# Kernel tuning notes

Hardware: AMD Instinct MI355X
Metric: run time of the kernel (lower is better)

Reference implementation:

```python
import jax, jax.numpy as jnp
import numpy as np

N, C_S, C_Z, H, D = 512, 384, 128, 16, 24  # c_hidden per head
EPS = 1e-5

def _ln(x, g, b):
    m = jnp.mean(x, axis=-1, keepdims=True)
    v = jnp.mean(jnp.square(x - m), axis=-1, keepdims=True)
    return (x - m) * jax.lax.rsqrt(v + EPS) * g + b

def setup_inputs() -> dict:
    key = jax.random.key(0)
    ks = jax.random.split(key, 12)
    s = lambda fan: 1.0 / np.sqrt(fan)
    return {
        "a": jax.random.normal(ks[0], (1, N, C_S), jnp.float32),
        "z": jax.random.normal(ks[1], (1, N, N, C_Z), jnp.float32),
        "g_a": jnp.ones((C_S,), jnp.float32),
        "b_a": jnp.zeros((C_S,), jnp.float32),
        "g_z": jnp.ones((C_Z,), jnp.float32),
        "b_z": jnp.zeros((C_Z,), jnp.float32),
        "Wz": jax.random.normal(ks[2], (C_Z, H), jnp.float32) * s(C_Z),
        "bz": jnp.zeros((H,), jnp.float32),
        "Wq": jax.random.normal(ks[3], (C_S, H * D), jnp.float32) * s(C_S),
        "Wk": jax.random.normal(ks[4], (C_S, H * D), jnp.float32) * s(C_S),
        "Wv": jax.random.normal(ks[5], (C_S, H * D), jnp.float32) * s(C_S),
        "Wg": jax.random.normal(ks[6], (C_S, H * D), jnp.float32) * s(C_S),
        "bg": jnp.zeros((H * D,), jnp.float32),
        "Wo": jax.random.normal(ks[7], (H * D, C_S), jnp.float32) * s(H * D),
        "bo": jnp.zeros((C_S,), jnp.float32),
    }

def reference(a, z, g_a, b_a, g_z, b_z, Wz, bz, Wq, Wk, Wv, Wg, bg, Wo, bo):
    B = a.shape[0]
    a_n = _ln(a, g_a, b_a)                       # [B,N,C_S]
    z_n = _ln(z, g_z, b_z)                       # [B,N,N,C_Z]
    # linear_z then permute(0,3,1,2): [B,N,N,H] -> [B,H,N,N]
    pair_bias = jnp.einsum('bijc,ch->bhij', z_n, Wz) + bz[None, :, None, None]
    q = (a_n @ Wq).reshape(B, N, H, D) * (1.0 / np.sqrt(D))
    k = (a_n @ Wk).reshape(B, N, H, D)
    v = (a_n @ Wv).reshape(B, N, H, D)
    scores = jnp.einsum('bqhd,bkhd->bhqk', q, k) + pair_bias
    p = jax.nn.softmax(scores, axis=-1)
    o = jnp.einsum('bhqk,bkhd->bqhd', p, v)      # [B,N,H,D]
    g = jax.nn.sigmoid(a_n @ Wg + bg).reshape(B, N, H, D)
    o = (o * g).reshape(B, N, H * D)
    return o @ Wo + bo                            # [B,N,C_S]
```

## Files before the change

### kernel.cpp

```cpp
#include <hip/hip_runtime.h>
#include <math.h>

#define N 512
#define CS 384
#define CZ 128
#define NH 16
#define DH 24
#define HD 384
#define NN (N*N)
#define EPS 1e-5f

#define OFF_AN   0
#define OFF_QT   196608
#define OFF_KT   393216
#define OFF_VT   589824
#define OFF_GT   786432
#define OFF_OG   983040
#define OFF_WZ2  1179648
#define OFF_SH   1181696
#define OFF_BH   1181712
#define OFF_BIAS 1181728

__global__ void __launch_bounds__(256) ln_prep_kernel(const float* __restrict__ a, const float* __restrict__ g_a,
                                                      const float* __restrict__ b_a, float* __restrict__ an_out,
                                                      const float* __restrict__ g_z, const float* __restrict__ lnb_z,
                                                      const float* __restrict__ Wz, const float* __restrict__ bz,
                                                      float* __restrict__ wz2, float* __restrict__ sh,
                                                      float* __restrict__ bh) {
    __shared__ float ls[NH][17], lb[NH][17];
    __shared__ float l1[4], l2[4];
    const int t = threadIdx.x;
    if (blockIdx.x == 256) {
        for (int i = t; i < NH * CZ; i += 256) {
            int h = i >> 7, c = i & (CZ - 1);
            wz2[h * CZ + c] = g_z[c] * Wz[c * NH + h];
        }
        int h = t >> 4, seg = t & 15;
        float s = 0.f, b = 0.f;
        #pragma unroll
        for (int i = 0; i < 8; ++i) {
            int c = seg * 8 + i;
            float w = Wz[c * NH + h];
            s += g_z[c] * w;
            b += lnb_z[c] * w;
        }
        ls[h][seg] = s; lb[h][seg] = b;
        __syncthreads();
        if (t < NH) {
            float ss = 0.f, bb = 0.f;
            #pragma unroll
            for (int i = 0; i < 16; ++i) { ss += ls[t][i]; bb += lb[t][i]; }
            sh[t] = ss;
            bh[t] = bb + bz[t];
        }
        return;
    }
    const int half = t >> 7;
    const int tr = t & 127;
    const int r = blockIdx.x * 2 + half;
    const float* row = a + r * CS;
    float x0 = row[tr], x1 = row[tr + 128], x2 = row[tr + 256];
    float s1 = x0 + x1 + x2;
    float s2 = x0 * x0 + x1 * x1 + x2 * x2;
    #pragma unroll
    for (int m = 1; m < 64; m <<= 1) {
        s1 += __shfl_xor(s1, m, 64);
        s2 += __shfl_xor(s2, m, 64);
    }
    if ((t & 63) == 0) { l1[t >> 6] = s1; l2[t >> 6] = s2; }
    __syncthreads();
    s1 = l1[half * 2] + l1[half * 2 + 1];
    s2 = l2[half * 2] + l2[half * 2 + 1];
    float mu = s1 * (1.f / CS);
    float var = s2 * (1.f / CS) - mu * mu;
    float rs = rsqrtf(var + EPS);
    float* an = an_out + r * CS;
    an[tr]       = (x0 - mu) * rs * g_a[tr]       + b_a[tr];
    an[tr + 128] = (x1 - mu) * rs * g_a[tr + 128] + b_a[tr + 128];
    an[tr + 256] = (x2 - mu) * rs * g_a[tr + 256] + b_a[tr + 256];
}

__global__ void __launch_bounds__(256) qkvg_kernel(const float* __restrict__ Wq, const float* __restrict__ Wk,
                                                   const float* __restrict__ Wv, const float* __restrict__ Wg,
                                                   const float* __restrict__ bg, const float* __restrict__ an,
                                                   float* __restrict__ qt, float* __restrict__ kt,
                                                   float* __restrict__ vt, float* __restrict__ gt) {
    const int lane = threadIdx.x & 63;
    const int w = __builtin_amdgcn_readfirstlane(threadIdx.x >> 6);
    const int strip = blockIdx.x * 4 + w;
    const int n0 = strip * 8;
    const int sel = n0 / HD;
    const int col = n0 % HD;
    const float* Wm = (sel == 0) ? Wq : (sel == 1) ? Wk : (sel == 2) ? Wv : Wg;
    const int m = blockIdx.y * 64 + lane;
    const float* arow = an + m * CS;
    float acc[8];
    #pragma unroll
    for (int j = 0; j < 8; ++j) acc[j] = 0.f;
    for (int kb = 0; kb < CS; kb += 32) {
        float4 av[8];
        #pragma unroll
        for (int i = 0; i < 8; ++i) av[i] = ((const float4*)(arow + kb))[i];
        #pragma unroll
        for (int i = 0; i < 8; ++i) {
            const float* wr = Wm + (kb + i * 4) * HD + col;
            #pragma unroll
            for (int j = 0; j < 8; ++j) {
                acc[j] += av[i].x * wr[j];
                acc[j] += av[i].y * wr[HD + j];
                acc[j] += av[i].z * wr[2 * HD + j];
                acc[j] += av[i].w * wr[3 * HD + j];
            }
        }
    }
    float* dst = (sel == 0) ? qt : (sel == 1) ? kt : (sel == 2) ? vt : gt;
    if (sel == 3) {
        #pragma unroll
        for (int j = 0; j < 8; ++j) acc[j] = 1.f / (1.f + __expf(-(acc[j] + bg[col + j])));
    } else if (sel == 0) {
        #pragma unroll
        for (int j = 0; j < 8; ++j) acc[j] *= 0.20412414523193153f;
    }
    #pragma unroll
    for (int j = 0; j < 8; ++j) {
        int c = col + j;
        int h = c / DH, d = c % DH;
        dst[(h * N + m) * DH + d] = acc[j];
    }
}

__global__ void __launch_bounds__(256, 4) pairbias_kernel(const float* __restrict__ z,
                                                          const float* __restrict__ wz2,
                                                          const float* __restrict__ sh,
                                                          const float* __restrict__ bh,
                                                          float* __restrict__ bias) {
    __shared__ float4 lz[64 * 32];
    const int t = threadIdx.x;
    const int l = t & 63;
    const int w = __builtin_amdgcn_readfirstlane(t >> 6);
    const int h0 = w * 4;
    const int row0 = blockIdx.x * 64;

    const float4* zsrc = (const float4*)(z + (size_t)row0 * CZ);
    #pragma unroll
    for (int i = 0; i < 8; ++i) {
        const int g4 = i * 256 + t;
        float4 v = zsrc[g4];
        const int r = g4 >> 5, cc = g4 & 31;
        lz[r * 32 + (cc ^ (r & 31))] = v;
    }
    __syncthreads();

    const unsigned base = (unsigned)(l * 512 + ((l & 31) << 4));
    const char* lzb = (const char*)lz;
    float s1 = 0.f, s2 = 0.f;
    float dots[4];
    #pragma unroll
    for (int j = 0; j < 4; ++j) dots[j] = 0.f;
    #pragma unroll
    for (int cc = 0; cc < 32; ++cc) {
        float4 v = *(const float4*)(lzb + (base ^ (unsigned)(cc << 4)));
        s1 += v.x + v.y + v.z + v.w;
        s2 += v.x * v.x + v.y * v.y + v.z * v.z + v.w * v.w;
        #pragma unroll
        for (int j = 0; j < 4; ++j) {
            const float4 wv = ((const float4*)(wz2 + (h0 + j) * CZ))[cc];
            dots[j] += v.x * wv.x + v.y * wv.y + v.z * wv.z + v.w * wv.w;
        }
    }
    const float mu = s1 * (1.f / CZ);
    const float var = s2 * (1.f / CZ) - mu * mu;
    const float rr = rsqrtf(var + EPS);
    const int row = row0 + l;
    #pragma unroll
    for (int j = 0; j < 4; ++j)
        bias[(h0 + j) * NN + row] = rr * (dots[j] - mu * sh[h0 + j]) + bh[h0 + j];
}

__global__ void __launch_bounds__(256) attn_kernel(const float* __restrict__ qt, const float* __restrict__ kt,
                                                   const float* __restrict__ vt, const float* __restrict__ gt,
                                                   const float* __restrict__ bias, float* __restrict__ og) {
    const int lane = threadIdx.x & 63;
    const int w = __builtin_amdgcn_readfirstlane(threadIdx.x >> 6);
    const int qhalf = lane >> 5;
    const int klane = lane & 31;
    const int h = blockIdx.y;
    const int q = blockIdx.x * 8 + w * 2 + qhalf;
    const float* qT = qt + h * N * DH;
    const float* kT = kt + h * N * DH;
    const float* vT = vt + h * N * DH;

    float qv[DH];
    #pragma unroll
    for (int d6 = 0; d6 < 6; ++d6) {
        float4 t4 = ((const float4*)(qT + q * DH))[d6];
        qv[d6 * 4 + 0] = t4.x; qv[d6 * 4 + 1] = t4.y; qv[d6 * 4 + 2] = t4.z; qv[d6 * 4 + 3] = t4.w;
    }
    float sc[16];
    #pragma unroll
    for (int t = 0; t < 16; ++t) {
        const int kk = t * 32 + klane;
        const float4* kr = (const float4*)(kT + kk * DH);
        float4 k0 = kr[0], k1 = kr[1], k2 = kr[2], k3 = kr[3], k4 = kr[4], k5 = kr[5];
        float s = qv[0]*k0.x + qv[1]*k0.y + qv[2]*k0.z + qv[3]*k0.w
                + qv[4]*k1.x + qv[5]*k1.y + qv[6]*k1.z + qv[7]*k1.w
                + qv[8]*k2.x + qv[9]*k2.y + qv[10]*k2.z + qv[11]*k2.w
                + qv[12]*k3.x + qv[13]*k3.y + qv[14]*k3.z + qv[15]*k3.w
                + qv[16]*k4.x + qv[17]*k4.y + qv[18]*k4.z + qv[19]*k4.w
                + qv[20]*k5.x + qv[21]*k5.y + qv[22]*k5.z + qv[23]*k5.w;
        sc[t] = s + bias[h * NN + q * N + kk];
    }
    float mx = sc[0];
    #pragma unroll
    for (int t = 1; t < 16; ++t) mx = fmaxf(mx, sc[t]);
    #pragma unroll
    for (int m = 1; m < 32; m <<= 1) mx = fmaxf(mx, __shfl_xor(mx, m, 64));
    float sum = 0.f;
    #pragma unroll
    for (int t = 0; t < 16; ++t) { sc[t] = __expf(sc[t] - mx); sum += sc[t]; }
    #pragma unroll
    for (int m = 1; m < 32; m <<= 1) sum += __shfl_xor(sum, m, 64);
    float inv = 1.f / sum;
    #pragma unroll
    for (int t = 0; t < 16; ++t) sc[t] *= inv;
    float acc[DH];
    #pragma unroll
    for (int d = 0; d < DH; ++d) acc[d] = 0.f;
    #pragma unroll
    for (int t = 0; t < 16; ++t) {
        const int kk = t * 32 + klane;
        const float4* vr = (const float4*)(vT + kk * DH);
        float4 v0 = vr[0], v1 = vr[1], v2 = vr[2], v3 = vr[3], v4 = vr[4], v5 = vr[5];
        float p = sc[t];
        acc[0] += p*v0.x;  acc[1] += p*v0.y;  acc[2] += p*v0.z;  acc[3] += p*v0.w;
        acc[4] += p*v1.x;  acc[5] += p*v1.y;  acc[6] += p*v1.z;  acc[7] += p*v1.w;
        acc[8] += p*v2.x;  acc[9] += p*v2.y;  acc[10] += p*v2.z; acc[11] += p*v2.w;
        acc[12] += p*v3.x; acc[13] += p*v3.y; acc[14] += p*v3.z; acc[15] += p*v3.w;
        acc[16] += p*v4.x; acc[17] += p*v4.y; acc[18] += p*v4.z; acc[19] += p*v4.w;
        acc[20] += p*v5.x; acc[21] += p*v5.y; acc[22] += p*v5.z; acc[23] += p*v5.w;
    }
    #pragma unroll
    for (int m = 1; m < 32; m <<= 1) {
        #pragma unroll
        for (int d = 0; d < DH; ++d) acc[d] += __shfl_xor(acc[d], m, 64);
    }
    float o = 0.f;
    #pragma unroll
    for (int d = 0; d < DH; ++d) o = (klane == d) ? acc[d] : o;
    if (klane < DH) {
        float g = gt[h * N * DH + q * DH + klane];
        og[q * HD + h * DH + klane] = o * g;
    }
}

__global__ void __launch_bounds__(256) out_gemm_kernel(const float* __restrict__ Wo, const float* __restrict__ bo,
                                                       const float* __restrict__ og, float* __restrict__ out) {
    const int lane = threadIdx.x & 63;
    const int w = __builtin_amdgcn_readfirstlane(threadIdx.x >> 6);
    const int strip = blockIdx.x * 4 + w;
    const int c0 = strip * 4;
    const int m = blockIdx.y * 64 + lane;
    const float* orow = og + m * HD;
    float acc[4];
    #pragma unroll
    for (int j = 0; j < 4; ++j) acc[j] = 0.f;
    for (int kb = 0; kb < HD; kb += 32) {
        float4 av[8];
        #pragma unroll
        for (int i = 0; i < 8; ++i) av[i] = ((const float4*)(orow + kb))[i];
        #pragma unroll
        for (int i = 0; i < 8; ++i) {
            const float* wr = Wo + (kb + i * 4) * CS + c0;
            #pragma unroll
            for (int j = 0; j < 4; ++j) {
                acc[j] += av[i].x * wr[j];
                acc[j] += av[i].y * wr[CS + j];
                acc[j] += av[i].z * wr[2 * CS + j];
                acc[j] += av[i].w * wr[3 * CS + j];
            }
        }
    }
    #pragma unroll
    for (int j = 0; j < 4; ++j) out[m * CS + c0 + j] = acc[j] + bo[c0 + j];
}

extern "C" void kernel_launch(void* const* d_in, const int* in_sizes, int n_in,
                              void* d_out, int out_size, void* d_ws, size_t ws_size,
                              hipStream_t stream) {
    const float* a    = (const float*)d_in[0];
    const float* z    = (const float*)d_in[1];
    const float* g_a  = (const float*)d_in[2];
    const float* b_a  = (const float*)d_in[3];
    const float* g_z  = (const float*)d_in[4];
    const float* b_z  = (const float*)d_in[5];
    const float* Wz   = (const float*)d_in[6];
    const float* bz   = (const float*)d_in[7];
    const float* Wq   = (const float*)d_in[8];
    const float* Wk   = (const float*)d_in[9];
    const float* Wv   = (const float*)d_in[10];
    const float* Wg   = (const float*)d_in[11];
    const float* bg   = (const float*)d_in[12];
    const float* Wo   = (const float*)d_in[13];
    const float* bo   = (const float*)d_in[14];
    float* ws  = (float*)d_ws;
    float* out = (float*)d_out;

    float* an   = ws + OFF_AN;
    float* qt   = ws + OFF_QT;
    float* kt   = ws + OFF_KT;
    float* vt   = ws + OFF_VT;
    float* gt   = ws + OFF_GT;
    float* ogp  = ws + OFF_OG;
    float* wz2  = ws + OFF_WZ2;
    float* shp  = ws + OFF_SH;
    float* bhp  = ws + OFF_BH;
    float* bias = ws + OFF_BIAS;

    hipLaunchKernelGGL(ln_prep_kernel, dim3(257),    dim3(256), 0, stream,
                       a, g_a, b_a, an, g_z, b_z, Wz, bz, wz2, shp, bhp);
    hipLaunchKernelGGL(qkvg_kernel,    dim3(48, 8),  dim3(256), 0, stream,
                       Wq, Wk, Wv, Wg, bg, an, qt, kt, vt, gt);
    hipLaunchKernelGGL(pairbias_kernel, dim3(4096),  dim3(256), 0, stream,
                       z, wz2, shp, bhp, bias);
    hipLaunchKernelGGL(attn_kernel,    dim3(64, 16), dim3(256), 0, stream,
                       qt, kt, vt, gt, bias, ogp);
    hipLaunchKernelGGL(out_gemm_kernel, dim3(24, 8), dim3(256), 0, stream,
                       Wo, bo, ogp, out);
}
```

Baseline: 334.0 us.

## Merge QKVG projection into pair-bias kernel and shrink output GEMM strips

Combines the QKVG projection and the pair-bias computation into one launch. Every ninth block does a narrower 6-column projection strip and the other blocks do pair-bias rows, so the small compute-bound GEMM overlaps the bandwidth-bound z streaming. The output GEMM now computes 2 columns per wave over a 1D grid of 384 blocks, giving more blocks for better occupancy. This saves one launch and the idle tail between kernels, at the cost of branch divergence per block and less weight reuse per thread.

```diff
diff --git a/kernel.cpp b/kernel.cpp
--- a/kernel.cpp
+++ b/kernel.cpp
@@ -80,66 +80,69 @@
     an[tr + 256] = (x2 - mu) * rs * g_a[tr + 256] + b_a[tr + 256];
 }
 
-__global__ void __launch_bounds__(256) qkvg_kernel(const float* __restrict__ Wq, const float* __restrict__ Wk,
-                                                   const float* __restrict__ Wv, const float* __restrict__ Wg,
-                                                   const float* __restrict__ bg, const float* __restrict__ an,
-                                                   float* __restrict__ qt, float* __restrict__ kt,
-                                                   float* __restrict__ vt, float* __restrict__ gt) {
-    const int lane = threadIdx.x & 63;
-    const int w = __builtin_amdgcn_readfirstlane(threadIdx.x >> 6);
-    const int strip = blockIdx.x * 4 + w;
-    const int n0 = strip * 8;
-    const int sel = n0 / HD;
-    const int col = n0 % HD;
-    const float* Wm = (sel == 0) ? Wq : (sel == 1) ? Wk : (sel == 2) ? Wv : Wg;
-    const int m = blockIdx.y * 64 + lane;
-    const float* arow = an + m * CS;
-    float acc[8];
-    #pragma unroll
-    for (int j = 0; j < 8; ++j) acc[j] = 0.f;
-    for (int kb = 0; kb < CS; kb += 32) {
-        float4 av[8];
-        #pragma unroll
-        for (int i = 0; i < 8; ++i) av[i] = ((const float4*)(arow + kb))[i];
-        #pragma unroll
-        for (int i = 0; i < 8; ++i) {
-            const float* wr = Wm + (kb + i * 4) * HD + col;
-            #pragma unroll
-            for (int j = 0; j < 8; ++j) {
-                acc[j] += av[i].x * wr[j];
-                acc[j] += av[i].y * wr[HD + j];
-                acc[j] += av[i].z * wr[2 * HD + j];
-                acc[j] += av[i].w * wr[3 * HD + j];
+__global__ void __launch_bounds__(256, 4) qp2_kernel(const float* __restrict__ z,
+                                                     const float* __restrict__ wz2,
+                                                     const float* __restrict__ sh,
+                                                     const float* __restrict__ bh,
+                                                     float* __restrict__ bias,
+                                                     const float* __restrict__ Wq, const float* __restrict__ Wk,
+                                                     const float* __restrict__ Wv, const float* __restrict__ Wg,
+                                                     const float* __restrict__ bg, const float* __restrict__ an,
+                                                     float* __restrict__ qt, float* __restrict__ kt,
+                                                     float* __restrict__ vt, float* __restrict__ gt) {
+    __shared__ float4 lz[64 * 32];
+    const int b = blockIdx.x;
+    const int t = threadIdx.x;
+    const int lane = t & 63;
+    const int w = __builtin_amdgcn_readfirstlane(t >> 6);
+    if (b % 9 == 8) {
+        const int bq = b / 9;
+        const int wid = bq * 4 + w;
+        const int strip = wid >> 3;
+        const int mb = wid & 7;
+        const int n0 = strip * 6;
+        const int sel = n0 / HD;
+        const int col = n0 - sel * HD;
+        const float* Wm = (sel == 0) ? Wq : (sel == 1) ? Wk : (sel == 2) ? Wv : Wg;
+        const int m = mb * 64 + lane;
+        const float* arow = an + m * CS;
+        float acc[6];
+        #pragma unroll
+        for (int j = 0; j < 6; ++j) acc[j] = 0.f;
+        for (int kb = 0; kb < CS; kb += 32) {
+            float4 av[8];
+            #pragma unroll
+            for (int i = 0; i < 8; ++i) av[i] = ((const float4*)(arow + kb))[i];
+            #pragma unroll
+            for (int i = 0; i < 8; ++i) {
+                const float* wr = Wm + (kb + i * 4) * HD + col;
+                #pragma unroll
+                for (int j = 0; j < 6; ++j) {
+                    acc[j] += av[i].x * wr[j];
+                    acc[j] += av[i].y * wr[HD + j];
+                    acc[j] += av[i].z * wr[2 * HD + j];
+                    acc[j] += av[i].w * wr[3 * HD + j];
+                }
             }
         }
-    }
-    float* dst = (sel == 0) ? qt : (sel == 1) ? kt : (sel == 2) ? vt : gt;
-    if (sel == 3) {
-        #pragma unroll
-        for (int j = 0; j < 8; ++j) acc[j] = 1.f / (1.f + __expf(-(acc[j] + bg[col + j])));
-    } else if (sel == 0) {
-        #pragma unroll
-        for (int j = 0; j < 8; ++j) acc[j] *= 0.20412414523193153f;
-    }
-    #pragma unroll
-    for (int j = 0; j < 8; ++j) {
-        int c = col + j;
-        int h = c / DH, d = c % DH;
-        dst[(h * N + m) * DH + d] = acc[j];
-    }
-}
-
-__global__ void __launch_bounds__(256, 4) pairbias_kernel(const float* __restrict__ z,
-                                                          const float* __restrict__ wz2,
-                                                          const float* __restrict__ sh,
-                                                          const float* __restrict__ bh,
-                                                          float* __restrict__ bias) {
-    __shared__ float4 lz[64 * 32];
-    const int t = threadIdx.x;
+        float* dst = (sel == 0) ? qt : (sel == 1) ? kt : (sel == 2) ? vt : gt;
+        if (sel == 3) {
+            #pragma unroll
+            for (int j = 0; j < 6; ++j) acc[j] = 1.f / (1.f + __expf(-(acc[j] + bg[col + j])));
+        } else if (sel == 0) {
+            #pragma unroll
+            for (int j = 0; j < 6; ++j) acc[j] *= 0.20412414523193153f;
+        }
+        const int h = col / DH, d0 = col - h * DH;
+        float* dp = dst + (h * N + m) * DH + d0;
+        #pragma unroll
+        for (int j = 0; j < 6; ++j) dp[j] = acc[j];
+        return;
+    }
+    const int pb = b - (b + 1) / 9;
     const int l = t & 63;
-    const int w = __builtin_amdgcn_readfirstlane(t >> 6);
     const int h0 = w * 4;
-    const int row0 = blockIdx.x * 64;
+    const int row0 = pb * 64;
 
     const float4* zsrc = (const float4*)(z + (size_t)row0 * CZ);
     #pragma unroll
@@ -257,13 +260,14 @@
                                                        const float* __restrict__ og, float* __restrict__ out) {
     const int lane = threadIdx.x & 63;
     const int w = __builtin_amdgcn_readfirstlane(threadIdx.x >> 6);
-    const int strip = blockIdx.x * 4 + w;
-    const int c0 = strip * 4;
-    const int m = blockIdx.y * 64 + lane;
+    const int wid = blockIdx.x * 4 + w;
+    const int strip = wid >> 3;
+    const int mb = wid & 7;
+    const int c0 = strip * 2;
+    const int m = mb * 64 + lane;
     const float* orow = og + m * HD;
-    float acc[4];
-    #pragma unroll
-    for (int j = 0; j < 4; ++j) acc[j] = 0.f;
+    float acc[2];
+    acc[0] = 0.f; acc[1] = 0.f;
     for (int kb = 0; kb < HD; kb += 32) {
         float4 av[8];
         #pragma unroll
@@ -272,7 +276,7 @@
         for (int i = 0; i < 8; ++i) {
             const float* wr = Wo + (kb + i * 4) * CS + c0;
             #pragma unroll
-            for (int j = 0; j < 4; ++j) {
+            for (int j = 0; j < 2; ++j) {
                 acc[j] += av[i].x * wr[j];
                 acc[j] += av[i].y * wr[CS + j];
                 acc[j] += av[i].z * wr[2 * CS + j];
@@ -281,7 +285,7 @@
         }
     }
     #pragma unroll
-    for (int j = 0; j < 4; ++j) out[m * CS + c0 + j] = acc[j] + bo[c0 + j];
+    for (int j = 0; j < 2; ++j) out[m * CS + c0 + j] = acc[j] + bo[c0 + j];
 }
 
 extern "C" void kernel_launch(void* const* d_in, const int* in_sizes, int n_in,
@@ -318,12 +322,11 @@
 
     hipLaunchKernelGGL(ln_prep_kernel, dim3(257),    dim3(256), 0, stream,
                        a, g_a, b_a, an, g_z, b_z, Wz, bz, wz2, shp, bhp);
-    hipLaunchKernelGGL(qkvg_kernel,    dim3(48, 8),  dim3(256), 0, stream,
+    hipLaunchKernelGGL(qp2_kernel,     dim3(4608),   dim3(256), 0, stream,
+                       z, wz2, shp, bhp, bias,
                        Wq, Wk, Wv, Wg, bg, an, qt, kt, vt, gt);
-    hipLaunchKernelGGL(pairbias_kernel, dim3(4096),  dim3(256), 0, stream,
-                       z, wz2, shp, bhp, bias);
     hipLaunchKernelGGL(attn_kernel,    dim3(64, 16), dim3(256), 0, stream,
                        qt, kt, vt, gt, bias, ogp);
-    hipLaunchKernelGGL(out_gemm_kernel, dim3(24, 8), dim3(256), 0, stream,
+    hipLaunchKernelGGL(out_gemm_kernel, dim3(384),   dim3(256), 0, stream,
                        Wo, bo, ogp, out);
 }
```

Result: slower. 404.3 us (+21.0%).

## Stage K/V and GEMM activations in swizzled LDS, use online softmax in attention

Applied to the files above, without the earlier changes.

The attention kernel now loads 128-key tiles of K and V cooperatively into XOR-swizzled shared memory and uses an online (running max/sum) softmax across four tiles, instead of each wave reading K/V rows straight from global memory. The QKVG and output GEMMs stage the activation tile in swizzled LDS and halve the columns per wave, doubling the grid to raise parallelism. The intent is to cut redundant global loads and register pressure, at the cost of extra barriers and rescaling work per tile.

```diff
diff --git a/kernel.cpp b/kernel.cpp
--- a/kernel.cpp
+++ b/kernel.cpp
@@ -85,27 +85,38 @@
                                                    const float* __restrict__ bg, const float* __restrict__ an,
                                                    float* __restrict__ qt, float* __restrict__ kt,
                                                    float* __restrict__ vt, float* __restrict__ gt) {
-    const int lane = threadIdx.x & 63;
-    const int w = __builtin_amdgcn_readfirstlane(threadIdx.x >> 6);
-    const int strip = blockIdx.x * 4 + w;
-    const int n0 = strip * 8;
+    __shared__ float4 lan[64 * 8];
+    const int t = threadIdx.x;
+    const int lane = t & 63;
+    const int w = __builtin_amdgcn_readfirstlane(t >> 6);
+    const int s = blockIdx.x * 4 + w;
+    const int n0 = s * 4;
     const int sel = n0 / HD;
-    const int col = n0 % HD;
+    const int col = n0 - sel * HD;
     const float* Wm = (sel == 0) ? Wq : (sel == 1) ? Wk : (sel == 2) ? Wv : Wg;
-    const int m = blockIdx.y * 64 + lane;
-    const float* arow = an + m * CS;
-    float acc[8];
-    #pragma unroll
-    for (int j = 0; j < 8; ++j) acc[j] = 0.f;
+    const int m0 = blockIdx.y * 64;
+    const int m = m0 + lane;
+    const float4* an4 = (const float4*)an;
+    float acc[4];
+    #pragma unroll
+    for (int j = 0; j < 4; ++j) acc[j] = 0.f;
     for (int kb = 0; kb < CS; kb += 32) {
+        __syncthreads();
+        #pragma unroll
+        for (int i = 0; i < 2; ++i) {
+            const int idx = i * 256 + t;
+            const int r = idx >> 3, c = idx & 7;
+            lan[(r << 3) + (c ^ (r & 7))] = an4[(size_t)(m0 + r) * 96 + (kb >> 2) + c];
+        }
+        __syncthreads();
         float4 av[8];
         #pragma unroll
-        for (int i = 0; i < 8; ++i) av[i] = ((const float4*)(arow + kb))[i];
+        for (int i = 0; i < 8; ++i) av[i] = lan[(lane << 3) + (i ^ (lane & 7))];
         #pragma unroll
         for (int i = 0; i < 8; ++i) {
             const float* wr = Wm + (kb + i * 4) * HD + col;
             #pragma unroll
-            for (int j = 0; j < 8; ++j) {
+            for (int j = 0; j < 4; ++j) {
                 acc[j] += av[i].x * wr[j];
                 acc[j] += av[i].y * wr[HD + j];
                 acc[j] += av[i].z * wr[2 * HD + j];
@@ -116,17 +127,15 @@
     float* dst = (sel == 0) ? qt : (sel == 1) ? kt : (sel == 2) ? vt : gt;
     if (sel == 3) {
         #pragma unroll
-        for (int j = 0; j < 8; ++j) acc[j] = 1.f / (1.f + __expf(-(acc[j] + bg[col + j])));
+        for (int j = 0; j < 4; ++j) acc[j] = 1.f / (1.f + __expf(-(acc[j] + bg[col + j])));
     } else if (sel == 0) {
         #pragma unroll
-        for (int j = 0; j < 8; ++j) acc[j] *= 0.20412414523193153f;
-    }
-    #pragma unroll
-    for (int j = 0; j < 8; ++j) {
-        int c = col + j;
-        int h = c / DH, d = c % DH;
-        dst[(h * N + m) * DH + d] = acc[j];
-    }
+        for (int j = 0; j < 4; ++j) acc[j] *= 0.20412414523193153f;
+    }
+    const int h = col / DH, d0 = col - h * DH;
+    float* dp = dst + (h * N + m) * DH + d0;
+    #pragma unroll
+    for (int j = 0; j < 4; ++j) dp[j] = acc[j];
 }
 
 __global__ void __launch_bounds__(256, 4) pairbias_kernel(const float* __restrict__ z,
@@ -177,18 +186,22 @@
         bias[(h0 + j) * NN + row] = rr * (dots[j] - mu * sh[h0 + j]) + bh[h0 + j];
 }
 
-__global__ void __launch_bounds__(256) attn_kernel(const float* __restrict__ qt, const float* __restrict__ kt,
-                                                   const float* __restrict__ vt, const float* __restrict__ gt,
-                                                   const float* __restrict__ bias, float* __restrict__ og) {
-    const int lane = threadIdx.x & 63;
-    const int w = __builtin_amdgcn_readfirstlane(threadIdx.x >> 6);
+__global__ void __launch_bounds__(256, 4) attn_kernel(const float* __restrict__ qt, const float* __restrict__ kt,
+                                                      const float* __restrict__ vt, const float* __restrict__ gt,
+                                                      const float* __restrict__ bias, float* __restrict__ og) {
+    __shared__ float4 lzK[128 * 8];
+    __shared__ float4 lzV[128 * 8];
+    const int t = threadIdx.x;
+    const int lane = t & 63;
+    const int w = __builtin_amdgcn_readfirstlane(t >> 6);
     const int qhalf = lane >> 5;
     const int klane = lane & 31;
     const int h = blockIdx.y;
     const int q = blockIdx.x * 8 + w * 2 + qhalf;
     const float* qT = qt + h * N * DH;
-    const float* kT = kt + h * N * DH;
-    const float* vT = vt + h * N * DH;
+    const float4* kT4 = (const float4*)(kt + h * N * DH);
+    const float4* vT4 = (const float4*)(vt + h * N * DH);
+    const float* brow = bias + h * NN + q * N;
 
     float qv[DH];
     #pragma unroll
@@ -196,83 +209,115 @@
         float4 t4 = ((const float4*)(qT + q * DH))[d6];
         qv[d6 * 4 + 0] = t4.x; qv[d6 * 4 + 1] = t4.y; qv[d6 * 4 + 2] = t4.z; qv[d6 * 4 + 3] = t4.w;
     }
-    float sc[16];
-    #pragma unroll
-    for (int t = 0; t < 16; ++t) {
-        const int kk = t * 32 + klane;
-        const float4* kr = (const float4*)(kT + kk * DH);
-        float4 k0 = kr[0], k1 = kr[1], k2 = kr[2], k3 = kr[3], k4 = kr[4], k5 = kr[5];
-        float s = qv[0]*k0.x + qv[1]*k0.y + qv[2]*k0.z + qv[3]*k0.w
-                + qv[4]*k1.x + qv[5]*k1.y + qv[6]*k1.z + qv[7]*k1.w
-                + qv[8]*k2.x + qv[9]*k2.y + qv[10]*k2.z + qv[11]*k2.w
-                + qv[12]*k3.x + qv[13]*k3.y + qv[14]*k3.z + qv[15]*k3.w
-                + qv[16]*k4.x + qv[17]*k4.y + qv[18]*k4.z + qv[19]*k4.w
-                + qv[20]*k5.x + qv[21]*k5.y + qv[22]*k5.z + qv[23]*k5.w;
-        sc[t] = s + bias[h * NN + q * N + kk];
-    }
-    float mx = sc[0];
-    #pragma unroll
-    for (int t = 1; t < 16; ++t) mx = fmaxf(mx, sc[t]);
-    #pragma unroll
-    for (int m = 1; m < 32; m <<= 1) mx = fmaxf(mx, __shfl_xor(mx, m, 64));
-    float sum = 0.f;
-    #pragma unroll
-    for (int t = 0; t < 16; ++t) { sc[t] = __expf(sc[t] - mx); sum += sc[t]; }
-    #pragma unroll
-    for (int m = 1; m < 32; m <<= 1) sum += __shfl_xor(sum, m, 64);
-    float inv = 1.f / sum;
-    #pragma unroll
-    for (int t = 0; t < 16; ++t) sc[t] *= inv;
+    float m_run = -1e30f, l_run = 0.f;
     float acc[DH];
     #pragma unroll
     for (int d = 0; d < DH; ++d) acc[d] = 0.f;
-    #pragma unroll
-    for (int t = 0; t < 16; ++t) {
-        const int kk = t * 32 + klane;
-        const float4* vr = (const float4*)(vT + kk * DH);
-        float4 v0 = vr[0], v1 = vr[1], v2 = vr[2], v3 = vr[3], v4 = vr[4], v5 = vr[5];
-        float p = sc[t];
-        acc[0] += p*v0.x;  acc[1] += p*v0.y;  acc[2] += p*v0.z;  acc[3] += p*v0.w;
-        acc[4] += p*v1.x;  acc[5] += p*v1.y;  acc[6] += p*v1.z;  acc[7] += p*v1.w;
-        acc[8] += p*v2.x;  acc[9] += p*v2.y;  acc[10] += p*v2.z; acc[11] += p*v2.w;
-        acc[12] += p*v3.x; acc[13] += p*v3.y; acc[14] += p*v3.z; acc[15] += p*v3.w;
-        acc[16] += p*v4.x; acc[17] += p*v4.y; acc[18] += p*v4.z; acc[19] += p*v4.w;
-        acc[20] += p*v5.x; acc[21] += p*v5.y; acc[22] += p*v5.z; acc[23] += p*v5.w;
+
+    for (int tile = 0; tile < 4; ++tile) {
+        __syncthreads();
+        const int kt0 = tile * 128;
+        #pragma unroll
+        for (int i = 0; i < 3; ++i) {
+            const int idx = i * 256 + t;
+            const int r = idx / 6, c = idx - r * 6;
+            const int slot = (r << 3) + (c ^ (r & 7));
+            lzK[slot] = kT4[kt0 * 6 + idx];
+            lzV[slot] = vT4[kt0 * 6 + idx];
+        }
+        __syncthreads();
+        float sc[4];
+        #pragma unroll
+        for (int j = 0; j < 4; ++j) {
+            const int kk = j * 32 + klane;
+            const float4* kr = lzK + (kk << 3);
+            const int x = kk & 7;
+            float4 k0 = kr[0 ^ x], k1 = kr[1 ^ x], k2 = kr[2 ^ x],
+                   k3 = kr[3 ^ x], k4 = kr[4 ^ x], k5 = kr[5 ^ x];
+            float s = qv[0]*k0.x + qv[1]*k0.y + qv[2]*k0.z + qv[3]*k0.w
+                    + qv[4]*k1.x + qv[5]*k1.y + qv[6]*k1.z + qv[7]*k1.w
+                    + qv[8]*k2.x + qv[9]*k2.y + qv[10]*k2.z + qv[11]*k2.w
+                    + qv[12]*k3.x + qv[13]*k3.y + qv[14]*k3.z + qv[15]*k3.w
+                    + qv[16]*k4.x + qv[17]*k4.y + qv[18]*k4.z + qv[19]*k4.w
+                    + qv[20]*k5.x + qv[21]*k5.y + qv[22]*k5.z + qv[23]*k5.w;
+            sc[j] = s + brow[kt0 + kk];
+        }
+        float tm = fmaxf(fmaxf(sc[0], sc[1]), fmaxf(sc[2], sc[3]));
+        #pragma unroll
+        for (int m = 1; m < 32; m <<= 1) tm = fmaxf(tm, __shfl_xor(tm, m, 64));
+        const float m_new = fmaxf(m_run, tm);
+        const float scale = __expf(m_run - m_new);
+        l_run *= scale;
+        #pragma unroll
+        for (int d = 0; d < DH; ++d) acc[d] *= scale;
+        float p[4], ps = 0.f;
+        #pragma unroll
+        for (int j = 0; j < 4; ++j) { p[j] = __expf(sc[j] - m_new); ps += p[j]; }
+        #pragma unroll
+        for (int m = 1; m < 32; m <<= 1) ps += __shfl_xor(ps, m, 64);
+        l_run += ps;
+        m_run = m_new;
+        #pragma unroll
+        for (int j = 0; j < 4; ++j) {
+            const int kk = j * 32 + klane;
+            const float4* vr = lzV + (kk << 3);
+            const int x = kk & 7;
+            float4 v0 = vr[0 ^ x], v1 = vr[1 ^ x], v2 = vr[2 ^ x],
+                   v3 = vr[3 ^ x], v4 = vr[4 ^ x], v5 = vr[5 ^ x];
+            const float pj = p[j];
+            acc[0] += pj*v0.x;  acc[1] += pj*v0.y;  acc[2] += pj*v0.z;  acc[3] += pj*v0.w;
+            acc[4] += pj*v1.x;  acc[5] += pj*v1.y;  acc[6] += pj*v1.z;  acc[7] += pj*v1.w;
+            acc[8] += pj*v2.x;  acc[9] += pj*v2.y;  acc[10] += pj*v2.z; acc[11] += pj*v2.w;
+            acc[12] += pj*v3.x; acc[13] += pj*v3.y; acc[14] += pj*v3.z; acc[15] += pj*v3.w;
+            acc[16] += pj*v4.x; acc[17] += pj*v4.y; acc[18] += pj*v4.z; acc[19] += pj*v4.w;
+            acc[20] += pj*v5.x; acc[21] += pj*v5.y; acc[22] += pj*v5.z; acc[23] += pj*v5.w;
+        }
     }
     #pragma unroll
     for (int m = 1; m < 32; m <<= 1) {
         #pragma unroll
         for (int d = 0; d < DH; ++d) acc[d] += __shfl_xor(acc[d], m, 64);
     }
+    const float inv = 1.f / l_run;
     float o = 0.f;
     #pragma unroll
     for (int d = 0; d < DH; ++d) o = (klane == d) ? acc[d] : o;
     if (klane < DH) {
         float g = gt[h * N * DH + q * DH + klane];
-        og[q * HD + h * DH + klane] = o * g;
+        og[q * HD + h * DH + klane] = o * inv * g;
     }
 }
 
 __global__ void __launch_bounds__(256) out_gemm_kernel(const float* __restrict__ Wo, const float* __restrict__ bo,
                                                        const float* __restrict__ og, float* __restrict__ out) {
-    const int lane = threadIdx.x & 63;
-    const int w = __builtin_amdgcn_readfirstlane(threadIdx.x >> 6);
-    const int strip = blockIdx.x * 4 + w;
-    const int c0 = strip * 4;
-    const int m = blockIdx.y * 64 + lane;
-    const float* orow = og + m * HD;
-    float acc[4];
-    #pragma unroll
-    for (int j = 0; j < 4; ++j) acc[j] = 0.f;
+    __shared__ float4 lo[64 * 8];
+    const int t = threadIdx.x;
+    const int lane = t & 63;
+    const int w = __builtin_amdgcn_readfirstlane(t >> 6);
+    const int s = blockIdx.x * 4 + w;
+    const int c0 = s * 2;
+    const int m0 = blockIdx.y * 64;
+    const int m = m0 + lane;
+    const float4* og4 = (const float4*)og;
+    float acc[2];
+    acc[0] = 0.f; acc[1] = 0.f;
     for (int kb = 0; kb < HD; kb += 32) {
+        __syncthreads();
+        #pragma unroll
+        for (int i = 0; i < 2; ++i) {
+            const int idx = i * 256 + t;
+            const int r = idx >> 3, c = idx & 7;
+            lo[(r << 3) + (c ^ (r & 7))] = og4[(size_t)(m0 + r) * 96 + (kb >> 2) + c];
+        }
+        __syncthreads();
         float4 av[8];
         #pragma unroll
-        for (int i = 0; i < 8; ++i) av[i] = ((const float4*)(orow + kb))[i];
+        for (int i = 0; i < 8; ++i) av[i] = lo[(lane << 3) + (i ^ (lane & 7))];
         #pragma unroll
         for (int i = 0; i < 8; ++i) {
             const float* wr = Wo + (kb + i * 4) * CS + c0;
             #pragma unroll
-            for (int j = 0; j < 4; ++j) {
+            for (int j = 0; j < 2; ++j) {
                 acc[j] += av[i].x * wr[j];
                 acc[j] += av[i].y * wr[CS + j];
                 acc[j] += av[i].z * wr[2 * CS + j];
@@ -281,7 +326,7 @@
         }
     }
     #pragma unroll
-    for (int j = 0; j < 4; ++j) out[m * CS + c0 + j] = acc[j] + bo[c0 + j];
+    for (int j = 0; j < 2; ++j) out[m * CS + c0 + j] = acc[j] + bo[c0 + j];
 }
 
 extern "C" void kernel_launch(void* const* d_in, const int* in_sizes, int n_in,
@@ -318,12 +363,12 @@
 
     hipLaunchKernelGGL(ln_prep_kernel, dim3(257),    dim3(256), 0, stream,
                        a, g_a, b_a, an, g_z, b_z, Wz, bz, wz2, shp, bhp);
-    hipLaunchKernelGGL(qkvg_kernel,    dim3(48, 8),  dim3(256), 0, stream,
+    hipLaunchKernelGGL(qkvg_kernel,    dim3(96, 8),  dim3(256), 0, stream,
                        Wq, Wk, Wv, Wg, bg, an, qt, kt, vt, gt);
     hipLaunchKernelGGL(pairbias_kernel, dim3(4096),  dim3(256), 0, stream,
                        z, wz2, shp, bhp, bias);
     hipLaunchKernelGGL(attn_kernel,    dim3(64, 16), dim3(256), 0, stream,
                        qt, kt, vt, gt, bias, ogp);
-    hipLaunchKernelGGL(out_gemm_kernel, dim3(24, 8), dim3(256), 0, stream,
+    hipLaunchKernelGGL(out_gemm_kernel, dim3(48, 8), dim3(256), 0, stream,
                        Wo, bo, ogp, out);
 }
```

After: 333.8 us. About the same (-0.1%).
